# Kernel optimization log

Measured on AMD Instinct MI355X. Metric: run time of the kernel, lower is better.

Reference implementation:

```python
import jax, jax.numpy as jnp
import numpy as np

DIM = 256
D_INNER = 512      # expand=2 * dim
D_STATE = 16
D_CONV = 4
DT_RANK = 16       # ceil(dim/16)
EPS = 1e-5


def _mamba_params(key):
    ks = jax.random.split(key, 6)
    s = lambda k, shape, fan: jax.random.normal(k, shape, jnp.float32) * (fan ** -0.5)
    in_w = s(ks[0], (2 * D_INNER, DIM), DIM)
    conv_w = s(ks[1], (D_INNER, 1, D_CONV), D_CONV)
    conv_b = jnp.zeros((D_INNER,), jnp.float32)
    xproj_w = s(ks[2], (DT_RANK + 2 * D_STATE, D_INNER), D_INNER)
    dt_w = s(ks[3], (D_INNER, DT_RANK), DT_RANK)
    # dt bias: inverse-softplus of dt sampled in [1e-3, 0.1] (mamba init)
    dt = jnp.exp(jax.random.uniform(ks[4], (D_INNER,)) * (np.log(0.1) - np.log(1e-3)) + np.log(1e-3))
    dt_b = jnp.log(jnp.expm1(dt))
    A_log = jnp.log(jnp.broadcast_to(jnp.arange(1, D_STATE + 1, dtype=jnp.float32), (D_INNER, D_STATE)))
    Dp = jnp.ones((D_INNER,), jnp.float32)
    out_w = s(ks[5], (DIM, D_INNER), D_INNER)
    return in_w, conv_w, conv_b, xproj_w, dt_w, dt_b, A_log, Dp, out_w


def _layernorm(x, w, b):
    mu = x.mean(-1, keepdims=True)
    var = ((x - mu) ** 2).mean(-1, keepdims=True)  # biased var (torch WithBias_LayerNorm)
    return (x - mu) / jnp.sqrt(var + EPS) * w + b


def _mamba(x, in_w, conv_w, conv_b, xproj_w, dt_w, dt_b, A_log, Dp, out_w):
    B, L, _ = x.shape
    xz = x @ in_w.T                      # (B, L, 2*d_inner)
    u, z = jnp.split(xz, 2, axis=-1)
    # causal depthwise conv1d (torch pads both sides then slices [:L] == left pad)
    uc = jnp.transpose(u, (0, 2, 1))     # (B, d_inner, L)
    uc = jax.lax.conv_general_dilated(uc, conv_w, (1,), [(D_CONV - 1, 0)],
                                      dimension_numbers=('NCH', 'OIH', 'NCH'),
                                      feature_group_count=D_INNER) + conv_b[None, :, None]
    u = jax.nn.silu(jnp.transpose(uc, (0, 2, 1)))          # (B, L, d_inner)
    dbl = u @ xproj_w.T
    dt, Bm, Cm = jnp.split(dbl, [DT_RANK, DT_RANK + D_STATE], axis=-1)
    delta = jax.nn.softplus(dt @ dt_w.T + dt_b)            # (B, L, d_inner)
    A = -jnp.exp(A_log)                                    # (d_inner, d_state)

    def step(h, inp):
        d_t, b_t, c_t, u_t = inp         # (B,di),(B,ds),(B,ds),(B,di)
        h = h * jnp.exp(d_t[..., None] * A) + (d_t * u_t)[..., None] * b_t[:, None, :]
        y = jnp.einsum('bds,bs->bd', h, c_t)
        return h, y

    h0 = jnp.zeros((B, D_INNER, D_STATE), jnp.float32)
    xs = (jnp.moveaxis(delta, 1, 0), jnp.moveaxis(Bm, 1, 0),
          jnp.moveaxis(Cm, 1, 0), jnp.moveaxis(u, 1, 0))
    _, ys = jax.lax.scan(step, h0, xs)
    y = jnp.moveaxis(ys, 0, 1) + u * Dp
    y = y * jax.nn.silu(z)
    return y @ out_w.T


def setup_inputs() -> dict:
    key = jax.random.key(0)
    ks = jax.random.split(key, 4)
    B, N = 16, 2048
    x1 = jax.random.normal(ks[0], (B, N, DIM), jnp.float32)
    x2 = jax.random.normal(ks[1], (B, N, DIM), jnp.float32)
    ratio = jnp.float32(0.5)  # nn.Parameter init_ratio
    ln1_w = jnp.ones((DIM,), jnp.float32); ln1_b = jnp.zeros((DIM,), jnp.float32)
    ln2_w = jnp.ones((DIM,), jnp.float32); ln2_b = jnp.zeros((DIM,), jnp.float32)
    e1 = _mamba_params(ks[2]); e2 = _mamba_params(ks[3])
    names = ['in_w', 'conv_w', 'conv_b', 'xproj_w', 'dt_w', 'dt_b', 'A_log', 'D', 'out_w']
    d = {'x1': x1, 'x2': x2, 'ratio': ratio,
         'ln1_w': ln1_w, 'ln1_b': ln1_b, 'ln2_w': ln2_w, 'ln2_b': ln2_b}
    d.update({f'e1_{n}': v for n, v in zip(names, e1)})
    d.update({f'e2_{n}': v for n, v in zip(names, e2)})
    return d


def reference(x1, x2, ratio, ln1_w, ln1_b, ln2_w, ln2_b,
              e1_in_w, e1_conv_w, e1_conv_b, e1_xproj_w, e1_dt_w, e1_dt_b, e1_A_log, e1_D, e1_out_w,
              e2_in_w, e2_conv_w, e2_conv_b, e2_xproj_w, e2_dt_w, e2_dt_b, e2_A_log, e2_D, e2_out_w):
    # torch: num_chans = int(C * sigmoid(ratio)) -> static shape decision (int() severs grad)
    nc = int(DIM / (1.0 + np.exp(-np.asarray(ratio, dtype=np.float32))))
    x1_short, x2_short = x1, x2
    x1n = _layernorm(x1, ln1_w, ln1_b)
    x2n = _layernorm(x2, ln2_w, ln2_b)
    # faithful to torch: x1 is overwritten first, then x2 reads from the NEW x1
    x1s = jnp.concatenate([x2n[:, :, :nc], x1n[:, :, nc:]], axis=2)
    x2s = jnp.concatenate([x1s[:, :, :nc], x2n[:, :, nc:]], axis=2)
    o1 = _mamba(x1s, e1_in_w, e1_conv_w, e1_conv_b, e1_xproj_w, e1_dt_w, e1_dt_b, e1_A_log, e1_D, e1_out_w) + x1_short
    o2 = _mamba(x2s, e2_in_w, e2_conv_w, e2_conv_b, e2_xproj_w, e2_dt_w, e2_dt_b, e2_A_log, e2_D, e2_out_w) + x2_short
    return (o1, o2)
```

## Files before the change

### kernel.cpp

```cpp
#include <hip/hip_runtime.h>

typedef unsigned short ushort_t;
typedef __attribute__((ext_vector_type(8))) short bh8;
typedef __attribute__((ext_vector_type(4))) float f32x4;
typedef __attribute__((ext_vector_type(2))) unsigned int u32x2;
typedef __attribute__((ext_vector_type(4))) unsigned int u32x4;

#define DIM 256
#define DI 512
#define LEN 2048
#define BATCH 16
#define NROW (BATCH * LEN)
#define NCHUNK (NROW / 8)

__device__ __forceinline__ float b2f(ushort_t u) {
    union { unsigned int i; float f; } v; v.i = ((unsigned int)u) << 16; return v.f;
}
__device__ __forceinline__ ushort_t f2b(float f) {
    union { float ff; unsigned int i; } v; v.ff = f;
    unsigned int x = v.i;
    x += 0x7fffu + ((x >> 16) & 1u);
    return (ushort_t)(x >> 16);
}
__device__ __forceinline__ float fexp2(float x) { float r; asm("v_exp_f32 %0, %1" : "=v"(r) : "v"(x)); return r; }
__device__ __forceinline__ float flog2(float x) { float r; asm("v_log_f32 %0, %1" : "=v"(r) : "v"(x)); return r; }
__device__ __forceinline__ float frcp (float x) { float r; asm("v_rcp_f32 %0, %1" : "=v"(r) : "v"(x)); return r; }
__device__ __forceinline__ unsigned int cvtpk(float lo, float hi) {
    unsigned int r; asm("v_cvt_pk_bf16_f32 %0, %1, %2" : "=v"(r) : "v"(lo), "v"(hi)); return r;
}
__device__ __forceinline__ float silu(float x) {
    return x * frcp(1.0f + fexp2(-1.44269504f * x));
}
__device__ __forceinline__ float bsum8(float v) {
    float t;
    asm("v_add_f32_dpp %0, %1, %1 quad_perm:[1,0,3,2] row_mask:0xf bank_mask:0xf" : "=v"(t) : "v"(v));
    asm("v_add_f32_dpp %0, %1, %1 quad_perm:[2,3,0,1] row_mask:0xf bank_mask:0xf" : "=v"(v) : "v"(t));
    asm("v_add_f32_dpp %0, %1, %1 row_half_mirror row_mask:0xf bank_mask:0xf" : "=v"(t) : "v"(v));
    return t;
}
__device__ __forceinline__ void gload16(const void* g, void* l) {
    __builtin_amdgcn_global_load_lds((const __attribute__((address_space(1))) unsigned int*)g,
                                     (__attribute__((address_space(3))) unsigned int*)l, 16, 0, 0);
}

__global__ __launch_bounds__(256) void ln_swap_kernel(
    const float* __restrict__ x1, const float* __restrict__ x2,
    const float* __restrict__ ratio,
    const float* __restrict__ ln1w, const float* __restrict__ ln1b,
    const float* __restrict__ ln2w, const float* __restrict__ ln2b,
    ushort_t* __restrict__ xs1, ushort_t* __restrict__ xs2) {
    const int w = threadIdx.x >> 6, lane = threadIdx.x & 63;
    const int m = blockIdx.x * 4 + w;
    const int c0 = lane * 4;
    const size_t off = (size_t)m * DIM + c0;
    const f32x4 v1 = *(const f32x4*)(x1 + off);
    const f32x4 v2 = *(const f32x4*)(x2 + off);
    float s1 = 0.f, q1 = 0.f, s2 = 0.f, q2 = 0.f;
    #pragma unroll
    for (int k = 0; k < 4; k++) {
        s1 += v1[k]; q1 += v1[k] * v1[k];
        s2 += v2[k]; q2 += v2[k] * v2[k];
    }
    #pragma unroll
    for (int o = 32; o; o >>= 1) {
        s1 += __shfl_xor(s1, o); q1 += __shfl_xor(q1, o);
        s2 += __shfl_xor(s2, o); q2 += __shfl_xor(q2, o);
    }
    const float inv = 1.0f / DIM;
    const float mu1 = s1 * inv, mu2 = s2 * inv;
    const float r1 = rsqrtf(q1 * inv - mu1 * mu1 + 1e-5f);
    const float r2 = rsqrtf(q2 * inv - mu2 * mu2 + 1e-5f);
    const int nc = (int)(DIM / (1.0f + expf(-ratio[0])));
    const f32x4 w1 = *(const f32x4*)(ln1w + c0), b1 = *(const f32x4*)(ln1b + c0);
    const f32x4 w2 = *(const f32x4*)(ln2w + c0), b2 = *(const f32x4*)(ln2b + c0);
    float n1[4], n2[4], o1v[4];
    #pragma unroll
    for (int k = 0; k < 4; k++) {
        n1[k] = (v1[k] - mu1) * r1 * w1[k] + b1[k];
        n2[k] = (v2[k] - mu2) * r2 * w2[k] + b2[k];
        o1v[k] = (c0 + k < nc) ? n2[k] : n1[k];
    }
    u32x2 p2, p1;
    p2[0] = cvtpk(n2[0], n2[1]);  p2[1] = cvtpk(n2[2], n2[3]);
    p1[0] = cvtpk(o1v[0], o1v[1]); p1[1] = cvtpk(o1v[2], o1v[3]);
    *(u32x2*)(&xs2[off]) = p2;
    *(u32x2*)(&xs1[off]) = p1;
}

#define WB_IN 0
#define WB_XP 262144
#define WB_OUT 286720
#define WB_TOT 417792
__global__ __launch_bounds__(256) void cvtw_kernel(
    const float* __restrict__ iw0, const float* __restrict__ iw1,
    const float* __restrict__ xw0, const float* __restrict__ xw1,
    const float* __restrict__ ow0, const float* __restrict__ ow1,
    ushort_t* __restrict__ o0, ushort_t* __restrict__ o1) {
    const int e = blockIdx.z;
    const float* iw = e ? iw1 : iw0;
    const float* xw = e ? xw1 : xw0;
    const float* ow = e ? ow1 : ow0;
    ushort_t* o = e ? o1 : o0;
    const int idx = blockIdx.x * 256 + threadIdx.x;
    if (idx < WB_XP) o[idx] = f2b(iw[idx]);
    else if (idx < WB_OUT) o[idx] = f2b(xw[idx - WB_XP]);
    else if (idx < WB_TOT) o[idx] = f2b(ow[idx - WB_OUT]);
}

__global__ __launch_bounds__(256) void gemm_in_kernel(
    const ushort_t* __restrict__ A0, const ushort_t* __restrict__ A1,
    const ushort_t* __restrict__ Wb0, const ushort_t* __restrict__ Wb1,
    ushort_t* __restrict__ uT0, ushort_t* __restrict__ uT1,
    ushort_t* __restrict__ zT0, ushort_t* __restrict__ zT1) {
    const int e = blockIdx.z;
    const ushort_t* __restrict__ A = e ? A1 : A0;
    const ushort_t* __restrict__ W = e ? Wb1 : Wb0;
    ushort_t* __restrict__ uT = e ? uT1 : uT0;
    ushort_t* __restrict__ zT = e ? zT1 : zT0;
    const int g = blockIdx.x;
    const int xcd = g & 7;
    const int idx = g >> 3;
    const int n0 = (idx & 7) * 128;
    const int m0 = (xcd * 32 + (idx >> 3)) * 128;
    const int tid = threadIdx.x, lane = tid & 63, wv = tid >> 6;
    const int wr = wv >> 1, wc = wv & 1;

    __shared__ ushort_t sA[128 * 32];
    __shared__ ushort_t sW[128 * 32];

    f32x4 acc[4][4];
    #pragma unroll
    for (int i = 0; i < 4; i++)
        #pragma unroll
        for (int j = 0; j < 4; j++) acc[i][j] = (f32x4){0.f, 0.f, 0.f, 0.f};

    const ushort_t* Ap = A + (size_t)(m0 + wv * 32 + (lane >> 2)) * 256 + (lane & 3) * 8;
    const ushort_t* Wp = W + (size_t)(n0 + wv * 32 + (lane >> 2)) * 256 + (lane & 3) * 8;

    for (int kt = 0; kt < 256; kt += 32) {
        __syncthreads();
        gload16(Ap + kt,             &sA[(wv * 32) * 32]);
        gload16(Ap + kt + 16 * 256,  &sA[(wv * 32 + 16) * 32]);
        gload16(Wp + kt,             &sW[(wv * 32) * 32]);
        gload16(Wp + kt + 16 * 256,  &sW[(wv * 32 + 16) * 32]);
        __syncthreads();
        bh8 af[4], wf[4];
        #pragma unroll
        for (int i = 0; i < 4; i++)
            af[i] = *(const bh8*)(&sA[(wr * 64 + i * 16 + (lane & 15)) * 32 + (lane >> 4) * 8]);
        #pragma unroll
        for (int j = 0; j < 4; j++)
            wf[j] = *(const bh8*)(&sW[(wc * 64 + j * 16 + (lane & 15)) * 32 + (lane >> 4) * 8]);
        #pragma unroll
        for (int i = 0; i < 4; i++)
            #pragma unroll
            for (int j = 0; j < 4; j++)
                acc[i][j] = __builtin_amdgcn_mfma_f32_16x16x32_bf16(af[i], wf[j], acc[i][j], 0, 0, 0);
    }

    #pragma unroll
    for (int i = 0; i < 4; i++) {
        #pragma unroll
        for (int j = 0; j < 4; j++) {
            const int rbase = m0 + wr * 64 + i * 16 + (lane >> 4) * 4;
            const int col = n0 + wc * 64 + j * 16 + (lane & 15);
            u32x2 vv;
            vv[0] = cvtpk(acc[i][j][0], acc[i][j][1]);
            vv[1] = cvtpk(acc[i][j][2], acc[i][j][3]);
            if (col < DI) *(u32x2*)(&uT[(size_t)col * NROW + rbase]) = vv;
            else          *(u32x2*)(&zT[(size_t)(col - DI) * NROW + rbase]) = vv;
        }
    }
}

__global__ __launch_bounds__(256) void conv_silu_kernel(
    const ushort_t* __restrict__ uT0, const ushort_t* __restrict__ uT1,
    const float* __restrict__ cw0, const float* __restrict__ cw1,
    const float* __restrict__ cb0, const float* __restrict__ cb1,
    ushort_t* __restrict__ ucT0, ushort_t* __restrict__ ucT1) {
    const int e = blockIdx.z;
    const ushort_t* __restrict__ uT = e ? uT1 : uT0;
    const float* __restrict__ cw = e ? cw1 : cw0;
    const float* __restrict__ cb = e ? cb1 : cb0;
    ushort_t* __restrict__ ucT = e ? ucT1 : ucT0;

    const int g = blockIdx.x * 256 + threadIdx.x;
    const int c = g & (NCHUNK - 1);
    const int d = g >> 12;
    const int b = c >> 8;
    const int t0 = (c & 255) * 8;
    const size_t base = (size_t)d * NROW + b * LEN + t0;

    bh8 cur = *(const bh8*)(uT + base);
    float win[11];
    if (t0) {
        win[0] = b2f(uT[base - 3]); win[1] = b2f(uT[base - 2]); win[2] = b2f(uT[base - 1]);
    } else {
        win[0] = 0.f; win[1] = 0.f; win[2] = 0.f;
    }
    #pragma unroll
    for (int j = 0; j < 8; j++) win[3 + j] = b2f((ushort_t)cur[j]);
    const f32x4 w = *(const f32x4*)(cw + d * 4);
    const float bias = cb[d];
    float s[8];
    #pragma unroll
    for (int j = 0; j < 8; j++) {
        const float a = bias + w[0] * win[j] + w[1] * win[j + 1] + w[2] * win[j + 2] + w[3] * win[j + 3];
        s[j] = silu(a);
    }
    u32x4 o;
    #pragma unroll
    for (int k = 0; k < 4; k++) o[k] = cvtpk(s[2 * k], s[2 * k + 1]);
    *(u32x4*)(ucT + base) = o;
}

__global__ __launch_bounds__(256) void gemm_xp_kernel(
    const ushort_t* __restrict__ ucT0, const ushort_t* __restrict__ ucT1,
    const ushort_t* __restrict__ Wb0, const ushort_t* __restrict__ Wb1,
    float* __restrict__ dbl0, float* __restrict__ dbl1,
    float* __restrict__ BCt0, float* __restrict__ BCt1) {
    const int e = blockIdx.z;
    const ushort_t* __restrict__ ucT = e ? ucT1 : ucT0;
    const ushort_t* __restrict__ W = (e ? Wb1 : Wb0) + WB_XP;
    float* __restrict__ dbl = e ? dbl1 : dbl0;
    float* __restrict__ BCt = e ? BCt1 : BCt0;
    const int m0 = blockIdx.x * 128;
    const int tid = threadIdx.x, lane = tid & 63;
    const int wc = tid >> 6;

    __shared__ ushort_t sW[48 * 40];
    __shared__ ushort_t sB[128 * 40];

    f32x4 acc[3][2];
    #pragma unroll
    for (int i = 0; i < 3; i++)
        #pragma unroll
        for (int j = 0; j < 2; j++) acc[i][j] = (f32x4){0.f, 0.f, 0.f, 0.f};

    const int kk = tid >> 3, mc = (tid & 7) * 16;
    const ushort_t* Bp = ucT + (size_t)kk * NROW + m0 + mc;

    for (int kt = 0; kt < 512; kt += 32) {
        __syncthreads();
        if (tid < 192) {
            const int r = tid >> 2, cc = (tid & 3) * 8;
            bh8 v = *(const bh8*)(W + (size_t)r * 512 + kt + cc);
            *(bh8*)(&sW[r * 40 + cc]) = v;
        }
        bh8 a0 = *(const bh8*)(Bp + (size_t)kt * NROW);
        bh8 a1 = *(const bh8*)(Bp + (size_t)kt * NROW + 8);
        #pragma unroll
        for (int q = 0; q < 8; q++) {
            sB[(mc + q) * 40 + kk] = (ushort_t)a0[q];
            sB[(mc + 8 + q) * 40 + kk] = (ushort_t)a1[q];
        }
        __syncthreads();
        bh8 af[3], wf[2];
        #pragma unroll
        for (int i = 0; i < 3; i++)
            af[i] = *(const bh8*)(&sW[(i * 16 + (lane & 15)) * 40 + (lane >> 4) * 8]);
        #pragma unroll
        for (int j = 0; j < 2; j++)
            wf[j] = *(const bh8*)(&sB[(wc * 32 + j * 16 + (lane & 15)) * 40 + (lane >> 4) * 8]);
        #pragma unroll
        for (int i = 0; i < 3; i++)
            #pragma unroll
            for (int j = 0; j < 2; j++)
                acc[i][j] = __builtin_amdgcn_mfma_f32_16x16x32_bf16(af[i], wf[j], acc[i][j], 0, 0, 0);
    }

    #pragma unroll
    for (int j = 0; j < 2; j++) {
        const int mm = m0 + wc * 32 + j * 16 + (lane & 15);
        {
            const int nb = (lane >> 4) * 4;
            #pragma unroll
            for (int r = 0; r < 4; r++)
                dbl[(size_t)(nb + r) * NROW + mm] = acc[0][j][r];
        }
        #pragma unroll
        for (int i = 1; i < 3; i++) {
            #pragma unroll
            for (int r = 0; r < 4; r++) {
                const int sigma = (lane >> 4) * 4 + r;
                const int pos = ((sigma & 7) << 2) + (sigma >> 3) + ((i == 2) ? 2 : 0);
                BCt[(size_t)mm * 32 + pos] = acc[i][j][r];
            }
        }
    }
}

__global__ __launch_bounds__(256) void delta_kernel(
    const float* __restrict__ dblT0, const float* __restrict__ dblT1,
    const float* __restrict__ dtw0, const float* __restrict__ dtw1,
    const float* __restrict__ dtb0, const float* __restrict__ dtb1,
    ushort_t* __restrict__ delT0, ushort_t* __restrict__ delT1) {
    const int e = blockIdx.z;
    const float* __restrict__ dblT = e ? dblT1 : dblT0;
    const float* __restrict__ dtw = e ? dtw1 : dtw0;
    const float* __restrict__ dtb = e ? dtb1 : dtb0;
    ushort_t* __restrict__ delT = e ? delT1 : delT0;

    const int tid = threadIdx.x, lane = tid & 63, wv = tid >> 6;
    const int bx = blockIdx.x;
    const int d = (bx & 127) * 4 + wv;
    const int m0 = (bx >> 7) * 256 + lane * 4;

    const float bias = dtb[d];
    f32x4 acc = {bias, bias, bias, bias};
    #pragma unroll
    for (int k = 0; k < 16; k++) {
        const float wk = dtw[d * 16 + k];
        const f32x4 bv = *(const f32x4*)(dblT + (size_t)k * NROW + m0);
        #pragma unroll
        for (int c = 0; c < 4; c++) acc[c] = fmaf(wk, bv[c], acc[c]);
    }
    float sp[4];
    #pragma unroll
    for (int c = 0; c < 4; c++) {
        const float x = acc[c];
        sp[c] = (x > 20.0f) ? x : 0.69314718f * flog2(1.0f + fexp2(1.44269504f * x));
    }
    u32x2 r;
    r[0] = cvtpk(sp[0], sp[1]);
    r[1] = cvtpk(sp[2], sp[3]);
    *(u32x2*)(&delT[(size_t)d * NROW + m0]) = r;
}

__global__ __launch_bounds__(256) void scan_kernel(
    const ushort_t* delT0, const ushort_t* delT1,
    const ushort_t* __restrict__ ucT0, const ushort_t* __restrict__ ucT1,
    const float* __restrict__ BCt0, const float* __restrict__ BCt1,
    const float* __restrict__ al0, const float* __restrict__ al1,
    const float* __restrict__ Dp0, const float* __restrict__ Dp1,
    ushort_t* y0, ushort_t* y1) {
    const int gid = blockIdx.x;
    const int xcd = gid & 7;
    const int k = gid >> 3;
    const int combo = xcd * 4 + (k >> 4);
    const int dtile = k & 15;
    const int e = combo & 1;
    const int b = combo >> 1;

    const ushort_t* delT = e ? delT1 : delT0;
    const ushort_t* __restrict__ ucT = e ? ucT1 : ucT0;
    const float* __restrict__ BCt = e ? BCt1 : BCt0;
    const float* __restrict__ al = e ? al1 : al0;
    const float* __restrict__ Dq = e ? Dp1 : Dp0;
    ushort_t* yo = e ? y1 : y0;

    const int tid = threadIdx.x;
    const int w = tid >> 6, lane = tid & 63;
    const int sl = lane & 7;
    const int dloc = tid >> 3;
    const int d = dtile * 32 + dloc;

    __shared__ ushort_t sD[2][32 * 64];
    __shared__ ushort_t sU[2][32 * 64];
    __shared__ float sBC[2][64 * 32];

    const int srow = tid >> 3;
    const int scw = ((tid & 7) ^ (srow & 7)) * 8;
    const ushort_t* srcD = delT + (size_t)(dtile * 32 + srow) * NROW + b * LEN + scw;
    const ushort_t* srcU = ucT  + (size_t)(dtile * 32 + srow) * NROW + b * LEN + scw;
    const float* srcBC = BCt + (size_t)b * LEN * 32;

    const float A2a = -expf(al[(d << 4) + sl]) * 1.44269504f;
    const float A2b = -expf(al[(d << 4) + sl + 8]) * 1.44269504f;
    const float Dpv8 = Dq[d] * 0.125f;

    ushort_t* yp = yo + (size_t)d * NROW + b * LEN;

    gload16(srcD, &sD[0][srow * 64 + (tid & 7) * 8]);
    gload16(srcU, &sU[0][srow * 64 + (tid & 7) * 8]);
    gload16(srcBC + (w * 2 + 0) * 256 + lane * 4, &sBC[0][(w * 2 + 0) * 256]);
    gload16(srcBC + (w * 2 + 1) * 256 + lane * 4, &sBC[0][(w * 2 + 1) * 256]);
    __syncthreads();

    float h0 = 0.f, h1 = 0.f;
    for (int sup = 0; sup < 32; sup++) {
        const int q = sup & 1;
        {
            gload16(srcD + (sup + 1) * 64, &sD[q ^ 1][srow * 64 + (tid & 7) * 8]);
            gload16(srcU + (sup + 1) * 64, &sU[q ^ 1][srow * 64 + (tid & 7) * 8]);
            const float* sb = srcBC + (size_t)(sup + 1) * 2048;
            gload16(sb + (w * 2 + 0) * 256 + lane * 4, &sBC[q ^ 1][(w * 2 + 0) * 256]);
            gload16(sb + (w * 2 + 1) * 256 + lane * 4, &sBC[q ^ 1][(w * 2 + 1) * 256]);
        }
        #pragma unroll
        for (int sub = 0; sub < 8; sub++) {
            const int sw = ((sub ^ (dloc & 7)) << 3);
            const bh8 dv = *(const bh8*)(&sD[q][dloc * 64 + sw]);
            const bh8 uv = *(const bh8*)(&sU[q][dloc * 64 + sw]);
            float yv[8];
            #pragma unroll
            for (int j = 0; j < 8; j++) {
                const int t = sub * 8 + j;
                const float dt = b2f((ushort_t)dv[j]);
                const float uf = b2f((ushort_t)uv[j]);
                const float dtuf = dt * uf;
                const f32x4 bc = *(const f32x4*)(&sBC[q][t * 32 + sl * 4]);
                h0 = fmaf(h0, fexp2(dt * A2a), dtuf * bc[0]);
                h1 = fmaf(h1, fexp2(dt * A2b), dtuf * bc[1]);
                yv[j] = fmaf(uf, Dpv8, fmaf(h1, bc[3], h0 * bc[2]));
            }
            #pragma unroll
            for (int j = 0; j < 8; j++) yv[j] = bsum8(yv[j]);
            u32x4 o;
            #pragma unroll
            for (int kk = 0; kk < 4; kk++)
                o[kk] = cvtpk(yv[2 * kk], yv[2 * kk + 1]);
            if (sl == 0) *(u32x4*)(yp + sup * 64 + sub * 8) = o;
        }
        __syncthreads();
    }
}

__global__ __launch_bounds__(512) void gemm_out_kernel(
    const ushort_t* __restrict__ yT0, const ushort_t* __restrict__ yT1,
    const ushort_t* __restrict__ zT0, const ushort_t* __restrict__ zT1,
    const ushort_t* __restrict__ Wb0, const ushort_t* __restrict__ Wb1,
    const float* __restrict__ r0, const float* __restrict__ r1,
    float* __restrict__ o0, float* __restrict__ o1) {
    const int e = blockIdx.z;
    const ushort_t* __restrict__ yT = e ? yT1 : yT0;
    const ushort_t* __restrict__ zT = e ? zT1 : zT0;
    const ushort_t* __restrict__ W = (e ? Wb1 : Wb0) + WB_OUT;
    const float* __restrict__ rr = e ? r1 : r0;
    float* __restrict__ oo = e ? o1 : o0;
    const int m0 = blockIdx.x * 128;
    const int tid = threadIdx.x, lane = tid & 63, wv = tid >> 6;
    const int wr = wv & 1, wc = wv >> 1;

    __shared__ ushort_t sA[128 * 40];
    __shared__ ushort_t sW[256 * 32];

    f32x4 acc[4][4];
    #pragma unroll
    for (int i = 0; i < 4; i++)
        #pragma unroll
        for (int j = 0; j < 4; j++) acc[i][j] = (f32x4){0.f, 0.f, 0.f, 0.f};

    const int kk = tid >> 3, mc = (tid & 7) * 16;
    const ushort_t* Yp = yT + (size_t)kk * NROW + m0 + mc;
    const ushort_t* Zp = zT + (size_t)kk * NROW + m0 + mc;
    const int wq = (wv >= 4) ? (wv - 4) : 0;
    const ushort_t* Wp = W + (size_t)(wq * 64 + (lane >> 2)) * 512 + (lane & 3) * 8;

    for (int kt = 0; kt < 512; kt += 32) {
        __syncthreads();
        if (wv >= 4) {
            #pragma unroll
            for (int i = 0; i < 4; i++)
                gload16(Wp + kt + (size_t)i * 16 * 512, &sW[(wq * 64 + i * 16) * 32]);
        } else {
            bh8 a0 = *(const bh8*)(Yp + (size_t)kt * NROW);
            bh8 a1 = *(const bh8*)(Yp + (size_t)kt * NROW + 8);
            bh8 z0 = *(const bh8*)(Zp + (size_t)kt * NROW);
            bh8 z1 = *(const bh8*)(Zp + (size_t)kt * NROW + 8);
            #pragma unroll
            for (int q = 0; q < 4; q++) {
                const unsigned int p0 = cvtpk(
                    b2f((ushort_t)a0[2 * q])     * silu(b2f((ushort_t)z0[2 * q])),
                    b2f((ushort_t)a0[2 * q + 1]) * silu(b2f((ushort_t)z0[2 * q + 1])));
                const unsigned int p1 = cvtpk(
                    b2f((ushort_t)a1[2 * q])     * silu(b2f((ushort_t)z1[2 * q])),
                    b2f((ushort_t)a1[2 * q + 1]) * silu(b2f((ushort_t)z1[2 * q + 1])));
                sA[(mc + 2 * q) * 40 + kk]     = (ushort_t)p0;
                sA[(mc + 2 * q + 1) * 40 + kk] = (ushort_t)(p0 >> 16);
                sA[(mc + 8 + 2 * q) * 40 + kk]     = (ushort_t)p1;
                sA[(mc + 8 + 2 * q + 1) * 40 + kk] = (ushort_t)(p1 >> 16);
            }
        }
        __syncthreads();
        bh8 af[4], wf[4];
        #pragma unroll
        for (int i = 0; i < 4; i++)
            af[i] = *(const bh8*)(&sA[(wr * 64 + i * 16 + (lane & 15)) * 40 + (lane >> 4) * 8]);
        #pragma unroll
        for (int j = 0; j < 4; j++)
            wf[j] = *(const bh8*)(&sW[(wc * 64 + j * 16 + (lane & 15)) * 32 + (lane >> 4) * 8]);
        #pragma unroll
        for (int i = 0; i < 4; i++)
            #pragma unroll
            for (int j = 0; j < 4; j++)
                acc[i][j] = __builtin_amdgcn_mfma_f32_16x16x32_bf16(af[i], wf[j], acc[i][j], 0, 0, 0);
    }

    #pragma unroll
    for (int i = 0; i < 4; i++) {
        #pragma unroll
        for (int j = 0; j < 4; j++) {
            const int rbase = m0 + wr * 64 + i * 16 + (lane >> 4) * 4;
            const int col = wc * 64 + j * 16 + (lane & 15);
            #pragma unroll
            for (int r = 0; r < 4; r++) {
                const size_t off = (size_t)(rbase + r) * DIM + col;
                oo[off] = acc[i][j][r] + rr[off];
            }
        }
    }
}

extern "C" void kernel_launch(void* const* d_in, const int* in_sizes, int n_in,
                              void* d_out, int out_size, void* d_ws, size_t ws_size,
                              hipStream_t stream) {
    const float* x1    = (const float*)d_in[0];
    const float* x2    = (const float*)d_in[1];
    const float* ratio = (const float*)d_in[2];
    const float* ln1w  = (const float*)d_in[3];
    const float* ln1b  = (const float*)d_in[4];
    const float* ln2w  = (const float*)d_in[5];
    const float* ln2b  = (const float*)d_in[6];
    const float* inw[2]   = {(const float*)d_in[7],  (const float*)d_in[16]};
    const float* convw[2] = {(const float*)d_in[8],  (const float*)d_in[17]};
    const float* convb[2] = {(const float*)d_in[9],  (const float*)d_in[18]};
    const float* xprw[2]  = {(const float*)d_in[10], (const float*)d_in[19]};
    const float* dtw[2]   = {(const float*)d_in[11], (const float*)d_in[20]};
    const float* dtb[2]   = {(const float*)d_in[12], (const float*)d_in[21]};
    const float* alog[2]  = {(const float*)d_in[13], (const float*)d_in[22]};
    const float* Dp[2]    = {(const float*)d_in[14], (const float*)d_in[23]};
    const float* outw[2]  = {(const float*)d_in[15], (const float*)d_in[24]};

    float* o1 = (float*)d_out;
    float* o2 = o1 + (size_t)NROW * DIM;
    ushort_t* xs[2] = {(ushort_t*)o1, (ushort_t*)o2};
    const size_t XS_BYTES  = (size_t)NROW * DIM * 2;
    const size_t DBL_BYTES = (size_t)16 * NROW * 4;
    float* dbl[2] = {(float*)((char*)o1 + XS_BYTES), (float*)((char*)o2 + XS_BYTES)};
    float* BCt[2] = {(float*)((char*)o1 + XS_BYTES + DBL_BYTES),
                     (float*)((char*)o2 + XS_BYTES + DBL_BYTES)};

    const size_t SZ_DI = (size_t)NROW * DI * 2;
    const size_t SZ_WB = ((size_t)WB_TOT * 2 + 255) & ~(size_t)255;
    char* p = (char*)d_ws;
    ushort_t* uT[2]  = {(ushort_t*)p, (ushort_t*)(p + SZ_DI)};            p += 2 * SZ_DI;
    ushort_t* zT[2]  = {(ushort_t*)p, (ushort_t*)(p + SZ_DI)};            p += 2 * SZ_DI;
    ushort_t* ucT[2] = {(ushort_t*)p, (ushort_t*)(p + SZ_DI)};            p += 2 * SZ_DI;
    ushort_t* wbf[2] = {(ushort_t*)p, (ushort_t*)(p + SZ_WB)};
    ushort_t* delT[2] = {uT[0], uT[1]};
    ushort_t* yT[2]   = {uT[0], uT[1]};

    ln_swap_kernel<<<NROW / 4, 256, 0, stream>>>(x1, x2, ratio, ln1w, ln1b, ln2w, ln2b, xs[0], xs[1]);

    cvtw_kernel<<<dim3(WB_TOT / 256, 1, 2), 256, 0, stream>>>(
        inw[0], inw[1], xprw[0], xprw[1], outw[0], outw[1], wbf[0], wbf[1]);

    gemm_in_kernel<<<dim3(2048, 1, 2), 256, 0, stream>>>(
        xs[0], xs[1], wbf[0], wbf[1], uT[0], uT[1], zT[0], zT[1]);

    conv_silu_kernel<<<dim3((DI * NCHUNK) / 256, 1, 2), 256, 0, stream>>>(
        uT[0], uT[1], convw[0], convw[1], convb[0], convb[1], ucT[0], ucT[1]);

    gemm_xp_kernel<<<dim3(NROW / 128, 1, 2), 256, 0, stream>>>(
        ucT[0], ucT[1], wbf[0], wbf[1], dbl[0], dbl[1], BCt[0], BCt[1]);

    delta_kernel<<<dim3(128 * 128, 1, 2), 256, 0, stream>>>(
        dbl[0], dbl[1], dtw[0], dtw[1], dtb[0], dtb[1], delT[0], delT[1]);

    scan_kernel<<<dim3(512), 256, 0, stream>>>(
        delT[0], delT[1], ucT[0], ucT[1], BCt[0], BCt[1],
        alog[0], alog[1], Dp[0], Dp[1], yT[0], yT[1]);

    gemm_out_kernel<<<dim3(NROW / 128, 1, 2), 512, 0, stream>>>(
        yT[0], yT[1], zT[0], zT[1], wbf[0], wbf[1], x1, x2, o1, o2);
}
```

Baseline: 452.3 us.

## Deepen scan prefetch to four buffers and spread out-GEMM loads across all waves

The selective-scan kernel moves from double to quad buffering in shared memory. It now stages two chunks ahead and processes two chunks per barrier, halving the __syncthreads count and giving loads more time to land. The output GEMM now has every wave load both W tiles and the gated y*silu(z) tile, instead of splitting waves into loader roles. This costs more LDS in the scan kernel, which may reduce occupancy, and the prefetch reads slightly further past each sequence's end.

```diff
diff --git a/kernel.cpp b/kernel.cpp
--- a/kernel.cpp
+++ b/kernel.cpp
@@ -355,9 +355,9 @@
     const int dloc = tid >> 3;
     const int d = dtile * 32 + dloc;
 
-    __shared__ ushort_t sD[2][32 * 64];
-    __shared__ ushort_t sU[2][32 * 64];
-    __shared__ float sBC[2][64 * 32];
+    __shared__ ushort_t sD[4][32 * 64];
+    __shared__ ushort_t sU[4][32 * 64];
+    __shared__ float sBC[4][64 * 32];
 
     const int srow = tid >> 3;
     const int scw = ((tid & 7) ^ (srow & 7)) * 8;
@@ -371,22 +371,16 @@
 
     ushort_t* yp = yo + (size_t)d * NROW + b * LEN;
 
-    gload16(srcD, &sD[0][srow * 64 + (tid & 7) * 8]);
-    gload16(srcU, &sU[0][srow * 64 + (tid & 7) * 8]);
-    gload16(srcBC + (w * 2 + 0) * 256 + lane * 4, &sBC[0][(w * 2 + 0) * 256]);
-    gload16(srcBC + (w * 2 + 1) * 256 + lane * 4, &sBC[0][(w * 2 + 1) * 256]);
-    __syncthreads();
-
     float h0 = 0.f, h1 = 0.f;
-    for (int sup = 0; sup < 32; sup++) {
-        const int q = sup & 1;
-        {
-            gload16(srcD + (sup + 1) * 64, &sD[q ^ 1][srow * 64 + (tid & 7) * 8]);
-            gload16(srcU + (sup + 1) * 64, &sU[q ^ 1][srow * 64 + (tid & 7) * 8]);
-            const float* sb = srcBC + (size_t)(sup + 1) * 2048;
-            gload16(sb + (w * 2 + 0) * 256 + lane * 4, &sBC[q ^ 1][(w * 2 + 0) * 256]);
-            gload16(sb + (w * 2 + 1) * 256 + lane * 4, &sBC[q ^ 1][(w * 2 + 1) * 256]);
-        }
+
+    auto STAGE = [&](int chunk, int buf) {
+        gload16(srcD + chunk * 64, &sD[buf][srow * 64 + (tid & 7) * 8]);
+        gload16(srcU + chunk * 64, &sU[buf][srow * 64 + (tid & 7) * 8]);
+        const float* sb = srcBC + (size_t)chunk * 2048;
+        gload16(sb + (w * 2 + 0) * 256 + lane * 4, &sBC[buf][(w * 2 + 0) * 256]);
+        gload16(sb + (w * 2 + 1) * 256 + lane * 4, &sBC[buf][(w * 2 + 1) * 256]);
+    };
+    auto COMPUTE = [&](int sup, int q) {
         #pragma unroll
         for (int sub = 0; sub < 8; sub++) {
             const int sw = ((sub ^ (dloc & 7)) << 3);
@@ -412,6 +406,18 @@
                 o[kk] = cvtpk(yv[2 * kk], yv[2 * kk + 1]);
             if (sl == 0) *(u32x4*)(yp + sup * 64 + sub * 8) = o;
         }
+    };
+
+    STAGE(0, 0);
+    STAGE(1, 1);
+    __syncthreads();
+
+    for (int p = 0; p < 16; p++) {
+        const int s0 = 2 * p, s1 = 2 * p + 1;
+        STAGE(s0 + 2, (s0 + 2) & 3);
+        STAGE(s1 + 2, (s1 + 2) & 3);
+        COMPUTE(s0, s0 & 3);
+        COMPUTE(s1, s1 & 3);
         __syncthreads();
     }
 }
@@ -441,35 +447,25 @@
         #pragma unroll
         for (int j = 0; j < 4; j++) acc[i][j] = (f32x4){0.f, 0.f, 0.f, 0.f};
 
-    const int kk = tid >> 3, mc = (tid & 7) * 16;
-    const ushort_t* Yp = yT + (size_t)kk * NROW + m0 + mc;
-    const ushort_t* Zp = zT + (size_t)kk * NROW + m0 + mc;
-    const int wq = (wv >= 4) ? (wv - 4) : 0;
-    const ushort_t* Wp = W + (size_t)(wq * 64 + (lane >> 2)) * 512 + (lane & 3) * 8;
+    const int kk2 = tid >> 4, mc2 = (tid & 15) * 8;
+    const ushort_t* Yp = yT + (size_t)kk2 * NROW + m0 + mc2;
+    const ushort_t* Zp = zT + (size_t)kk2 * NROW + m0 + mc2;
+    const ushort_t* Wp = W + (size_t)(wv * 32 + (lane >> 2)) * 512 + (lane & 3) * 8;
 
     for (int kt = 0; kt < 512; kt += 32) {
         __syncthreads();
-        if (wv >= 4) {
-            #pragma unroll
-            for (int i = 0; i < 4; i++)
-                gload16(Wp + kt + (size_t)i * 16 * 512, &sW[(wq * 64 + i * 16) * 32]);
-        } else {
+        gload16(Wp + kt,             &sW[(wv * 32) * 32]);
+        gload16(Wp + kt + 16 * 512,  &sW[(wv * 32 + 16) * 32]);
+        {
             bh8 a0 = *(const bh8*)(Yp + (size_t)kt * NROW);
-            bh8 a1 = *(const bh8*)(Yp + (size_t)kt * NROW + 8);
             bh8 z0 = *(const bh8*)(Zp + (size_t)kt * NROW);
-            bh8 z1 = *(const bh8*)(Zp + (size_t)kt * NROW + 8);
             #pragma unroll
             for (int q = 0; q < 4; q++) {
                 const unsigned int p0 = cvtpk(
                     b2f((ushort_t)a0[2 * q])     * silu(b2f((ushort_t)z0[2 * q])),
                     b2f((ushort_t)a0[2 * q + 1]) * silu(b2f((ushort_t)z0[2 * q + 1])));
-                const unsigned int p1 = cvtpk(
-                    b2f((ushort_t)a1[2 * q])     * silu(b2f((ushort_t)z1[2 * q])),
-                    b2f((ushort_t)a1[2 * q + 1]) * silu(b2f((ushort_t)z1[2 * q + 1])));
-                sA[(mc + 2 * q) * 40 + kk]     = (ushort_t)p0;
-                sA[(mc + 2 * q + 1) * 40 + kk] = (ushort_t)(p0 >> 16);
-                sA[(mc + 8 + 2 * q) * 40 + kk]     = (ushort_t)p1;
-                sA[(mc + 8 + 2 * q + 1) * 40 + kk] = (ushort_t)(p1 >> 16);
+                sA[(mc2 + 2 * q) * 40 + kk2]     = (ushort_t)p0;
+                sA[(mc2 + 2 * q + 1) * 40 + kk2] = (ushort_t)(p0 >> 16);
             }
         }
         __syncthreads();
```

After: 463.4 us. +2.5%, slower.
